# Kernel optimization log

Measured on AMD Instinct MI355X. Metric: run time of the kernel, lower is better.

## Reference

```python
import jax, jax.numpy as jnp
import numpy as np

OUT_SIZE = 14
CUTOFF = 0.2
VAR0 = 4            # var[0], mixin_factor = 0.0 -> current std = var[0]
BETA = 4.0
N_SQ = OUT_SIZE * OUT_SIZE
TAU = 0.5 / N_SQ
BATCH = 256
CHANNELS = 512


def _gkern_np(kernlen, std, vmin, vmax):
    n = np.arange(kernlen) - (kernlen - 1) / 2.0
    w = np.exp(-(n ** 2) / (2.0 * std * std))
    g = np.outer(w, w)
    return g * (vmax - vmin) + vmin


def _build_templates():
    n = OUT_SIZE
    base = _gkern_np(2 * n - 1, VAR0, -CUTOFF, 1.0)
    base = np.maximum(base, 0.0) * 2.0 - 1.0
    base = TAU * np.clip(BETA * base / n, -1.0, None)  # clamp(min=-1) only
    # unfold(0,n,1).unfold(1,n,1).reshape(-1,n,n) == sliding windows, row-major
    t = np.lib.stride_tricks.sliding_window_view(base, (n, n)).reshape(-1, n, n)
    t = np.flip(t, axis=0).copy()  # torch.flip(templates, dims=(0,))
    templates_f = jnp.asarray(t, jnp.float32)                    # (n^2, n, n)
    neg = -TAU * jnp.ones((1, n, n), jnp.float32)
    templates_b = jnp.concatenate([templates_f, neg], axis=0)    # (n^2+1, n, n)
    alpha = N_SQ / (1.0 + N_SQ)
    p_T = jnp.asarray(
        np.array([alpha / N_SQ] * N_SQ + [1.0 - alpha], np.float32))  # (n^2+1,)
    return templates_f, templates_b, p_T


def setup_inputs() -> dict:
    key = jax.random.key(0)
    templates_f, templates_b, p_T = _build_templates()
    x = jax.random.normal(key, (BATCH, CHANNELS, OUT_SIZE, OUT_SIZE), jnp.float32)
    return {"x": x, "templates_f": templates_f,
            "templates_b": templates_b, "p_T": p_T}


def reference(x, templates_f, templates_b, p_T):
    B, C, H, W = x.shape
    tau = 0.5 / (H * W)
    # max_pool2d with kernel == full spatial extent -> flat argmax per (b, c)
    idx = jnp.argmax(x.reshape(B, C, H * W), axis=-1)            # (B, C) int
    sel = templates_f[idx]                                       # (B, C, H, W)
    mask = sel / jnp.max(sel)                                    # global max
    mask = jax.nn.relu(mask - CUTOFF) / CUTOFF
    x_masked = x * mask
    # local loss (mutual-information style) on the masked activations
    tr_x_T = jnp.einsum('bcwh,twh->cbt', x_masked * tau, templates_b)  # (C,B,T)
    p_x_T = jax.nn.softmax(tr_x_T, axis=1)                       # softmax over b
    p_x = jnp.einsum('t,cbt->cb', p_T, p_x_T)                    # (C, B)
    log_ratio = jnp.log(p_x_T / p_x[:, :, None])                 # (C, B, T)
    p_x_T_log = jnp.einsum('cbt,cbt->ct', p_x_T, log_ratio)      # (C, T)
    loss = -jnp.einsum('t,ct->c', p_T, p_x_T_log)                # (C,)
    return x_masked, mask, loss
```

## Files before the change

kernel.cpp:

```cpp
#include <hip/hip_runtime.h>

#define BB 256
#define CCH 512
#define HW 196
#define TT 197
#define TROWS 208
#define TBK 224
#define KPAD 232

typedef __attribute__((ext_vector_type(8))) short bf16x8;
typedef __attribute__((ext_vector_type(4))) float f32x4;
typedef __attribute__((ext_vector_type(4))) unsigned short us4;

__device__ __forceinline__ unsigned short f2bf(float f) {
    union { float f; unsigned u; } v; v.f = f;
    unsigned r = v.u + 0x7FFFu + ((v.u >> 16) & 1u);
    return (unsigned short)(r >> 16);
}

__global__ void prep_gmax(const float* __restrict__ tf, float* __restrict__ wsf) {
    __shared__ float red[256];
    float m = -1e30f;
    for (int i = threadIdx.x; i < HW * HW; i += 256) m = fmaxf(m, tf[i]);
    red[threadIdx.x] = m;
    __syncthreads();
    for (int s = 128; s > 0; s >>= 1) {
        if (threadIdx.x < s) red[threadIdx.x] = fmaxf(red[threadIdx.x], red[threadIdx.x + s]);
        __syncthreads();
    }
    if (threadIdx.x == 0) wsf[0] = red[0];
}

__global__ void prep_tb(const float* __restrict__ tb, unsigned short* __restrict__ tb_bf) {
    int i = blockIdx.x * 256 + threadIdx.x;
    if (i >= TROWS * TBK) return;
    int r = i / TBK, k = i % TBK;
    const float tau = 0.5f / 196.0f;
    float v = (r < TT && k < HW) ? tb[r * HW + k] * tau : 0.0f;
    tb_bf[i] = f2bf(v);
}

extern "C" __global__ __launch_bounds__(1024)
void fused_main(const float* __restrict__ x, const float* __restrict__ tf,
                const float* __restrict__ pT, const unsigned short* __restrict__ tb_bf,
                const float* __restrict__ wsf,
                float* __restrict__ xm_out, float* __restrict__ mask_out,
                float* __restrict__ loss_out)
{
    extern __shared__ char smem[];
    unsigned short* X = (unsigned short*)smem;
    float* s_part = (float*)(smem + BB * KPAD * 2);
    float* rAs    = s_part + 16 * TROWS;
    float* pTs    = rAs + TROWS;
    float* red    = pTs + TROWS;

    const int c    = blockIdx.x;
    const int tid  = threadIdx.x;
    const int lane = tid & 63;
    const int w    = tid >> 6;
    const int l15  = lane & 15, lg = lane >> 4;
    const float rg = 1.0f / wsf[0];

    if (tid < TROWS) pTs[tid] = (tid < TT) ? pT[tid] : 0.0f;

    const int b = tid >> 2;
    const int q = tid & 3;
    const int nch = (q == 0) ? 13 : 12;

    const size_t rowoff = ((size_t)b * CCH + c) * HW;
    const float* xrow = x + rowoff;

    f32x4 xv[13];
    #pragma unroll
    for (int j = 0; j < 13; ++j)
        if (j < nch) xv[j] = *(const f32x4*)(xrow + (q + 4 * j) * 4);

    float bv = -1e30f; int bi = 0;
    #pragma unroll
    for (int j = 0; j < 13; ++j) if (j < nch) {
        #pragma unroll
        for (int e = 0; e < 4; ++e) {
            float v = xv[j][e];
            int k = (q + 4 * j) * 4 + e;
            if (v > bv) { bv = v; bi = k; }
        }
    }
    #pragma unroll
    for (int m = 1; m <= 2; m <<= 1) {
        float ov = __shfl_xor(bv, m, 64);
        int   oi = __shfl_xor(bi, m, 64);
        if (ov > bv || (ov == bv && oi < bi)) { bv = ov; bi = oi; }
    }

    const float* selrow = tf + (size_t)bi * HW;
    float* xmrow = xm_out + rowoff;
    float* mkrow = mask_out + rowoff;
    unsigned short* xr = X + b * KPAD;

    #pragma unroll
    for (int j = 0; j < 13; ++j) if (j < nch) {
        const int ch = q + 4 * j;
        f32x4 sel = *(const f32x4*)(selrow + ch * 4);
        f32x4 mk, xm;
        #pragma unroll
        for (int e = 0; e < 4; ++e) {
            float m = fmaxf(sel[e] * rg - 0.2f, 0.0f) * 5.0f;
            mk[e] = m;
            xm[e] = xv[j][e] * m;
        }
        *(f32x4*)(xmrow + ch * 4) = xm;
        *(f32x4*)(mkrow + ch * 4) = mk;
        us4 pk;
        #pragma unroll
        for (int e = 0; e < 4; ++e) pk[e] = f2bf(xm[e]);
        *(us4*)(xr + ch * 4) = pk;
    }
    if (q == 0) {
        #pragma unroll
        for (int j = 0; j < 9; ++j) {
            us4 z = (us4){0, 0, 0, 0};
            *(us4*)(xr + HW + 4 * j) = z;
        }
    }
    __syncthreads();

    f32x4 acc[13];
    #pragma unroll
    for (int mt = 0; mt < 13; ++mt) acc[mt] = (f32x4){0.f, 0.f, 0.f, 0.f};

    const unsigned short* xb = X + (w * 16 + l15) * KPAD;
    for (int kt = 0; kt < 7; ++kt) {
        const int kb = kt * 32 + lg * 8;
        bf16x8 bfrag = *(const bf16x8*)(xb + kb);
        #pragma unroll
        for (int mt = 0; mt < 13; ++mt) {
            bf16x8 afrag = *(const bf16x8*)(tb_bf + (mt * 16 + l15) * TBK + kb);
            acc[mt] = __builtin_amdgcn_mfma_f32_16x16x32_bf16(afrag, bfrag, acc[mt], 0, 0, 0);
        }
    }

    float* sp = s_part + w * TROWS;
    #pragma unroll
    for (int mt = 0; mt < 13; ++mt) {
        #pragma unroll
        for (int e = 0; e < 4; ++e) acc[mt][e] = __expf(acc[mt][e]);
        f32x4 s = acc[mt];
        #pragma unroll
        for (int m = 1; m <= 8; m <<= 1) {
            #pragma unroll
            for (int e = 0; e < 4; ++e) s[e] += __shfl_xor(s[e], m, 64);
        }
        if (l15 == 0) *(f32x4*)(sp + mt * 16 + lg * 4) = s;
    }
    __syncthreads();
    if (tid < TROWS) {
        float s = 0.f;
        #pragma unroll
        for (int w2 = 0; w2 < 16; ++w2) s += s_part[w2 * TROWS + tid];
        rAs[tid] = 1.0f / s;
    }
    __syncthreads();

    float px = 0.f;
    #pragma unroll
    for (int mt = 0; mt < 13; ++mt) {
        const int t0 = mt * 16 + lg * 4;
        f32x4 ra = *(const f32x4*)(rAs + t0);
        f32x4 pt = *(const f32x4*)(pTs + t0);
        #pragma unroll
        for (int e = 0; e < 4; ++e) {
            float p = acc[mt][e] * ra[e];
            acc[mt][e] = p;
            px += pt[e] * p;
        }
    }
    px += __shfl_xor(px, 16, 64);
    px += __shfl_xor(px, 32, 64);
    const float rpx = 1.0f / px;

    float part = 0.f;
    #pragma unroll
    for (int mt = 0; mt < 13; ++mt) {
        const int t0 = mt * 16 + lg * 4;
        f32x4 pt = *(const f32x4*)(pTs + t0);
        #pragma unroll
        for (int e = 0; e < 4; ++e) {
            float p = acc[mt][e];
            part += pt[e] * p * __logf(p * rpx);
        }
    }
    #pragma unroll
    for (int off = 32; off >= 1; off >>= 1) part += __shfl_xor(part, off, 64);
    if (lane == 0) red[w] = part;
    __syncthreads();
    if (tid == 0) {
        float s = 0.f;
        #pragma unroll
        for (int w2 = 0; w2 < 16; ++w2) s += red[w2];
        loss_out[c] = -s;
    }
}

extern "C" void kernel_launch(void* const* d_in, const int* in_sizes, int n_in,
                              void* d_out, int out_size, void* d_ws, size_t ws_size,
                              hipStream_t stream) {
    const float* x  = (const float*)d_in[0];
    const float* tf = (const float*)d_in[1];
    const float* tb = (const float*)d_in[2];
    const float* pT = (const float*)d_in[3];

    const size_t NOUT = (size_t)BB * CCH * HW;
    float* xm_out = (float*)d_out;
    float* mk_out = xm_out + NOUT;
    float* ls_out = mk_out + NOUT;

    float* wsf = (float*)d_ws;
    unsigned short* tb_bf = (unsigned short*)((char*)d_ws + 64);

    prep_gmax<<<1, 256, 0, stream>>>(tf, wsf);
    prep_tb<<<(TROWS * TBK + 255) / 256, 256, 0, stream>>>(tb, tb_bf);

    const size_t SMEM = (size_t)BB * KPAD * 2
                      + 16 * TROWS * 4
                      + TROWS * 4 + TROWS * 4 + 16 * 4;
    hipFuncSetAttribute((const void*)fused_main, hipFuncAttributeMaxDynamicSharedMemorySize, (int)SMEM);
    fused_main<<<dim3(CCH), dim3(1024), SMEM, stream>>>(x, tf, pT, tb_bf, wsf,
                                                        xm_out, mk_out, ls_out);
}
```

Before: 175.4 us.

## Split fused kernel into streaming mask pass and separate GEMM-loss pass

Splits the per-channel fused kernel into a fully coalesced streaming kernel that computes the argmax mask and writes x_masked and mask, then a GEMM/loss kernel that reads x_masked back from global memory and converts it to bf16 on the fly. The aim is to replace the strided per-channel reads of the old kernel (rows spread across the batch) with contiguous streaming, and to drop the large LDS staging buffer so occupancy can rise. The two prep kernels are merged into one launch. The cost is an extra read of x_masked (about 100MB) with strided access in the GEMM kernel, plus one more launch.

```diff
diff --git a/kernel.cpp b/kernel.cpp
--- a/kernel.cpp
+++ b/kernel.cpp
@@ -6,11 +6,9 @@
 #define TT 197
 #define TROWS 208
 #define TBK 224
-#define KPAD 232
 
 typedef __attribute__((ext_vector_type(8))) short bf16x8;
 typedef __attribute__((ext_vector_type(4))) float f32x4;
-typedef __attribute__((ext_vector_type(4))) unsigned short us4;
 
 __device__ __forceinline__ unsigned short f2bf(float f) {
     union { float f; unsigned u; } v; v.f = f;
@@ -18,123 +16,136 @@
     return (unsigned short)(r >> 16);
 }
 
-__global__ void prep_gmax(const float* __restrict__ tf, float* __restrict__ wsf) {
-    __shared__ float red[256];
-    float m = -1e30f;
-    for (int i = threadIdx.x; i < HW * HW; i += 256) m = fmaxf(m, tf[i]);
-    red[threadIdx.x] = m;
-    __syncthreads();
-    for (int s = 128; s > 0; s >>= 1) {
-        if (threadIdx.x < s) red[threadIdx.x] = fmaxf(red[threadIdx.x], red[threadIdx.x + s]);
+__global__ void prep(const float* __restrict__ tf, const float* __restrict__ tb,
+                     float* __restrict__ wsf, unsigned short* __restrict__ tb_bf) {
+    if (blockIdx.x < 182) {
+        int i = blockIdx.x * 256 + threadIdx.x;
+        int r = i / TBK, k = i % TBK;
+        const float tau = 0.5f / 196.0f;
+        float v = (r < TT && k < HW) ? tb[r * HW + k] * tau : 0.0f;
+        tb_bf[i] = f2bf(v);
+    } else {
+        __shared__ float red[256];
+        float m = -1e30f;
+        for (int i = threadIdx.x; i < HW * HW; i += 256) m = fmaxf(m, tf[i]);
+        red[threadIdx.x] = m;
         __syncthreads();
-    }
-    if (threadIdx.x == 0) wsf[0] = red[0];
-}
-
-__global__ void prep_tb(const float* __restrict__ tb, unsigned short* __restrict__ tb_bf) {
-    int i = blockIdx.x * 256 + threadIdx.x;
-    if (i >= TROWS * TBK) return;
-    int r = i / TBK, k = i % TBK;
-    const float tau = 0.5f / 196.0f;
-    float v = (r < TT && k < HW) ? tb[r * HW + k] * tau : 0.0f;
-    tb_bf[i] = f2bf(v);
+        for (int s = 128; s > 0; s >>= 1) {
+            if (threadIdx.x < s) red[threadIdx.x] = fmaxf(red[threadIdx.x], red[threadIdx.x + s]);
+            __syncthreads();
+        }
+        if (threadIdx.x == 0) wsf[0] = red[0];
+    }
+}
+
+extern "C" __global__ __launch_bounds__(256)
+void stream_mask(const float* __restrict__ x, const float* __restrict__ tf,
+                 const float* __restrict__ wsf,
+                 float* __restrict__ xm_out, float* __restrict__ mask_out)
+{
+    const int tid = threadIdx.x;
+    const int row = blockIdx.x * 64 + (tid >> 2);
+    const int q   = tid & 3;
+    const int nch = (q == 0) ? 13 : 12;
+    const float rg = 1.0f / wsf[0];
+
+    const size_t rowoff = (size_t)row * HW;
+    const float* xrow = x + rowoff;
+
+    f32x4 xv[13];
+    #pragma unroll
+    for (int j = 0; j < 13; ++j)
+        if (j < nch) xv[j] = *(const f32x4*)(xrow + (q + 4 * j) * 4);
+
+    float bv = -1e30f; int bi = 0;
+    #pragma unroll
+    for (int j = 0; j < 13; ++j) if (j < nch) {
+        #pragma unroll
+        for (int e = 0; e < 4; ++e) {
+            float v = xv[j][e];
+            int k = (q + 4 * j) * 4 + e;
+            if (v > bv) { bv = v; bi = k; }
+        }
+    }
+    #pragma unroll
+    for (int m = 1; m <= 2; m <<= 1) {
+        float ov = __shfl_xor(bv, m, 64);
+        int   oi = __shfl_xor(bi, m, 64);
+        if (ov > bv || (ov == bv && oi < bi)) { bv = ov; bi = oi; }
+    }
+
+    const float* selrow = tf + (size_t)bi * HW;
+    float* xmrow = xm_out + rowoff;
+    float* mkrow = mask_out + rowoff;
+
+    #pragma unroll
+    for (int j = 0; j < 13; ++j) if (j < nch) {
+        const int k0 = (q + 4 * j) * 4;
+        f32x4 sel = *(const f32x4*)(selrow + k0);
+        f32x4 mk, xm;
+        #pragma unroll
+        for (int e = 0; e < 4; ++e) {
+            float m = fmaxf(sel[e] * rg - 0.2f, 0.0f) * 5.0f;
+            mk[e] = m;
+            xm[e] = xv[j][e] * m;
+        }
+        *(f32x4*)(xmrow + k0) = xm;
+        *(f32x4*)(mkrow + k0) = mk;
+    }
 }
 
 extern "C" __global__ __launch_bounds__(1024)
-void fused_main(const float* __restrict__ x, const float* __restrict__ tf,
-                const float* __restrict__ pT, const unsigned short* __restrict__ tb_bf,
-                const float* __restrict__ wsf,
-                float* __restrict__ xm_out, float* __restrict__ mask_out,
-                float* __restrict__ loss_out)
+void gemm_loss(const float* __restrict__ xm, const unsigned short* __restrict__ tb_bf,
+               const float* __restrict__ pT, float* __restrict__ loss_out)
 {
-    extern __shared__ char smem[];
-    unsigned short* X = (unsigned short*)smem;
-    float* s_part = (float*)(smem + BB * KPAD * 2);
-    float* rAs    = s_part + 16 * TROWS;
-    float* pTs    = rAs + TROWS;
-    float* red    = pTs + TROWS;
+    __shared__ float s_part[16 * TROWS];
+    __shared__ float rAs[TROWS];
+    __shared__ float pTs[TROWS];
+    __shared__ float red[16];
 
     const int c    = blockIdx.x;
     const int tid  = threadIdx.x;
     const int lane = tid & 63;
     const int w    = tid >> 6;
     const int l15  = lane & 15, lg = lane >> 4;
-    const float rg = 1.0f / wsf[0];
 
     if (tid < TROWS) pTs[tid] = (tid < TT) ? pT[tid] : 0.0f;
 
-    const int b = tid >> 2;
-    const int q = tid & 3;
-    const int nch = (q == 0) ? 13 : 12;
-
-    const size_t rowoff = ((size_t)b * CCH + c) * HW;
-    const float* xrow = x + rowoff;
-
-    f32x4 xv[13];
-    #pragma unroll
-    for (int j = 0; j < 13; ++j)
-        if (j < nch) xv[j] = *(const f32x4*)(xrow + (q + 4 * j) * 4);
-
-    float bv = -1e30f; int bi = 0;
-    #pragma unroll
-    for (int j = 0; j < 13; ++j) if (j < nch) {
-        #pragma unroll
-        for (int e = 0; e < 4; ++e) {
-            float v = xv[j][e];
-            int k = (q + 4 * j) * 4 + e;
-            if (v > bv) { bv = v; bi = k; }
-        }
-    }
-    #pragma unroll
-    for (int m = 1; m <= 2; m <<= 1) {
-        float ov = __shfl_xor(bv, m, 64);
-        int   oi = __shfl_xor(bi, m, 64);
-        if (ov > bv || (ov == bv && oi < bi)) { bv = ov; bi = oi; }
-    }
-
-    const float* selrow = tf + (size_t)bi * HW;
-    float* xmrow = xm_out + rowoff;
-    float* mkrow = mask_out + rowoff;
-    unsigned short* xr = X + b * KPAD;
-
-    #pragma unroll
-    for (int j = 0; j < 13; ++j) if (j < nch) {
-        const int ch = q + 4 * j;
-        f32x4 sel = *(const f32x4*)(selrow + ch * 4);
-        f32x4 mk, xm;
-        #pragma unroll
-        for (int e = 0; e < 4; ++e) {
-            float m = fmaxf(sel[e] * rg - 0.2f, 0.0f) * 5.0f;
-            mk[e] = m;
-            xm[e] = xv[j][e] * m;
-        }
-        *(f32x4*)(xmrow + ch * 4) = xm;
-        *(f32x4*)(mkrow + ch * 4) = mk;
-        us4 pk;
-        #pragma unroll
-        for (int e = 0; e < 4; ++e) pk[e] = f2bf(xm[e]);
-        *(us4*)(xr + ch * 4) = pk;
-    }
-    if (q == 0) {
-        #pragma unroll
-        for (int j = 0; j < 9; ++j) {
-            us4 z = (us4){0, 0, 0, 0};
-            *(us4*)(xr + HW + 4 * j) = z;
-        }
-    }
-    __syncthreads();
+    const int b = w * 16 + l15;
+    const float* xrow = xm + ((size_t)b * CCH + c) * HW;
 
     f32x4 acc[13];
     #pragma unroll
     for (int mt = 0; mt < 13; ++mt) acc[mt] = (f32x4){0.f, 0.f, 0.f, 0.f};
 
-    const unsigned short* xb = X + (w * 16 + l15) * KPAD;
-    for (int kt = 0; kt < 7; ++kt) {
-        const int kb = kt * 32 + lg * 8;
-        bf16x8 bfrag = *(const bf16x8*)(xb + kb);
+    #pragma unroll 1
+    for (int kt = 0; kt < 6; ++kt) {
+        const int k0 = kt * 32 + lg * 8;
+        f32x4 u0 = *(const f32x4*)(xrow + k0);
+        f32x4 u1 = *(const f32x4*)(xrow + k0 + 4);
+        bf16x8 bfrag;
+        #pragma unroll
+        for (int e = 0; e < 4; ++e) {
+            bfrag[e]     = (short)f2bf(u0[e]);
+            bfrag[e + 4] = (short)f2bf(u1[e]);
+        }
         #pragma unroll
         for (int mt = 0; mt < 13; ++mt) {
-            bf16x8 afrag = *(const bf16x8*)(tb_bf + (mt * 16 + l15) * TBK + kb);
+            bf16x8 afrag = *(const bf16x8*)(tb_bf + (mt * 16 + l15) * TBK + k0);
+            acc[mt] = __builtin_amdgcn_mfma_f32_16x16x32_bf16(afrag, bfrag, acc[mt], 0, 0, 0);
+        }
+    }
+    {
+        const int k0 = 192 + lg * 8;
+        bf16x8 bfrag = (bf16x8){0, 0, 0, 0, 0, 0, 0, 0};
+        if (lg == 0) {
+            f32x4 u0 = *(const f32x4*)(xrow + 192);
+            #pragma unroll
+            for (int e = 0; e < 4; ++e) bfrag[e] = (short)f2bf(u0[e]);
+        }
+        #pragma unroll
+        for (int mt = 0; mt < 13; ++mt) {
+            bf16x8 afrag = *(const bf16x8*)(tb_bf + (mt * 16 + l15) * TBK + k0);
             acc[mt] = __builtin_amdgcn_mfma_f32_16x16x32_bf16(afrag, bfrag, acc[mt], 0, 0, 0);
         }
     }
@@ -217,13 +228,7 @@
     float* wsf = (float*)d_ws;
     unsigned short* tb_bf = (unsigned short*)((char*)d_ws + 64);
 
-    prep_gmax<<<1, 256, 0, stream>>>(tf, wsf);
-    prep_tb<<<(TROWS * TBK + 255) / 256, 256, 0, stream>>>(tb, tb_bf);
-
-    const size_t SMEM = (size_t)BB * KPAD * 2
-                      + 16 * TROWS * 4
-                      + TROWS * 4 + TROWS * 4 + 16 * 4;
-    hipFuncSetAttribute((const void*)fused_main, hipFuncAttributeMaxDynamicSharedMemorySize, (int)SMEM);
-    fused_main<<<dim3(CCH), dim3(1024), SMEM, stream>>>(x, tf, pT, tb_bf, wsf,
-                                                        xm_out, mk_out, ls_out);
-}
+    prep<<<183, 256, 0, stream>>>(tf, tb, wsf, tb_bf);
+    stream_mask<<<2048, 256, 0, stream>>>(x, tf, wsf, xm_out, mk_out);
+    gemm_loss<<<CCH, 1024, 0, stream>>>(xm_out, tb_bf, pT, ls_out);
+}
```

New measurement: 192.9 us. 10.0% more time.
